# Performance work log

Hardware: AMD Instinct MI355X
Metric: run time of the kernel (lower is better)

Reference implementation:

```python
import jax, jax.numpy as jnp
import numpy as np

N_EMB = 1024
HEAD_SIZE = 128


def setup_inputs() -> dict:
    key = jax.random.key(0)
    k1, k2, k3, k4 = jax.random.split(key, 4)
    B, T = 8, 4096
    x = jax.random.normal(k1, (B, T, N_EMB), dtype=jnp.float32)
    # nn.Linear(n_emb, head_size, bias=False) weights have shape [head_size, n_emb]
    s = 1.0 / np.sqrt(N_EMB)
    Wq = jax.random.uniform(k2, (HEAD_SIZE, N_EMB), jnp.float32, -s, s)
    Wk = jax.random.uniform(k3, (HEAD_SIZE, N_EMB), jnp.float32, -s, s)
    Wv = jax.random.uniform(k4, (HEAD_SIZE, N_EMB), jnp.float32, -s, s)
    return {"x": x, "Wq": Wq, "Wk": Wk, "Wv": Wv}


def reference(x, Wq, Wk, Wv):
    # x: [B, T, C]; W*: [H, C]
    B, T, C = x.shape
    H = Wq.shape[0]
    q = jnp.einsum('btc,hc->bth', x, Wq)
    k = jnp.einsum('btc,hc->bth', x, Wk)
    v = jnp.einsum('btc,hc->bth', x, Wv)
    scale = H ** -0.5
    wei = jnp.einsum('bth,bsh->bts', q, k) * scale  # [B, T, T]
    # causal mask: position t attends to s <= t
    causal = jnp.arange(T)[:, None] >= jnp.arange(T)[None, :]
    wei = jnp.where(causal, wei, -jnp.inf)
    wei = jax.nn.softmax(wei, axis=-1)
    # dropout treated as identity (eval mode)
    out = jnp.einsum('bts,bsh->bth', wei, v)  # [B, T, H]
    return out
```

## Files before the change

kernel.cpp:

```cpp
#include <hip/hip_runtime.h>
#include <hip/hip_bf16.h>

typedef __bf16 bf16_t;
typedef __attribute__((ext_vector_type(8))) __bf16 bf16x8;
typedef __attribute__((ext_vector_type(4))) __bf16 bf16x4;
typedef __attribute__((ext_vector_type(4))) float f32x4;

#define MFMA16(a, b, c) __builtin_amdgcn_mfma_f32_16x16x32_bf16((a), (b), (c), 0, 0, 0)

__device__ __forceinline__ void gload_lds16(const void* g, void* l) {
    __builtin_amdgcn_global_load_lds(
        (const __attribute__((address_space(1))) void*)g,
        (__attribute__((address_space(3))) void*)l, 16, 0, 0);
}

__global__ __launch_bounds__(256, 3) void proj_qkv(
    const float* __restrict__ X,
    const float* __restrict__ W0, const float* __restrict__ W1, const float* __restrict__ W2,
    bf16_t* __restrict__ O0, bf16_t* __restrict__ O1, bf16_t* __restrict__ O2)
{
    __shared__ __align__(16) char As[128 * 128];
    __shared__ __align__(16) char Bs[128 * 128];

    const int tid = threadIdx.x;
    const int wid = tid >> 6;
    const int lane = tid & 63;
    const int l15 = lane & 15, l4 = lane >> 4;
    const int wr = wid >> 1, wc = wid & 1;
    const int m0 = blockIdx.x * 128;

    const float* W = (blockIdx.y == 0) ? W0 : (blockIdx.y == 1 ? W1 : W2);

    const int r0 = tid >> 4;
    const int kq = tid & 15;
    const int swz = ((r0 & 7) << 4);

    f32x4 acc[4][4] = {};
    float4 xr[8];

    #pragma unroll
    for (int i = 0; i < 8; ++i)
        xr[i] = *(const float4*)(X + (size_t)(m0 + r0 + i * 16) * 1024 + kq * 4);

    for (int ks = 0; ks < 16; ++ks) {
        const int kb = ks * 64;
        #pragma unroll
        for (int i = 0; i < 8; ++i) {
            const int r = r0 + i * 16;
            bf16x4 av; av[0] = (bf16_t)xr[i].x; av[1] = (bf16_t)xr[i].y;
            av[2] = (bf16_t)xr[i].z; av[3] = (bf16_t)xr[i].w;
            *(bf16x4*)(As + r * 128 + ((kq * 8) ^ swz)) = av;
        }
        #pragma unroll
        for (int i = 0; i < 8; ++i) {
            const int r = r0 + i * 16;
            float4 wa = *(const float4*)(W + (size_t)r * 1024 + kb + kq * 4);
            bf16x4 wv; wv[0] = (bf16_t)wa.x; wv[1] = (bf16_t)wa.y;
            wv[2] = (bf16_t)wa.z; wv[3] = (bf16_t)wa.w;
            *(bf16x4*)(Bs + r * 128 + ((kq * 8) ^ swz)) = wv;
        }
        __syncthreads();
        if (ks < 15) {
            #pragma unroll
            for (int i = 0; i < 8; ++i)
                xr[i] = *(const float4*)(X + (size_t)(m0 + r0 + i * 16) * 1024 + kb + 64 + kq * 4);
        }
        #pragma unroll
        for (int kk = 0; kk < 64; kk += 32) {
            const int kbyte = 2 * kk + 16 * l4;
            bf16x8 af[4], bfr[4];
            #pragma unroll
            for (int mi = 0; mi < 4; ++mi) {
                int r = wr * 64 + mi * 16 + l15;
                af[mi] = *(const bf16x8*)(As + r * 128 + (kbyte ^ ((r & 7) << 4)));
            }
            #pragma unroll
            for (int ni = 0; ni < 4; ++ni) {
                int r = wc * 64 + ni * 16 + l15;
                bfr[ni] = *(const bf16x8*)(Bs + r * 128 + (kbyte ^ ((r & 7) << 4)));
            }
            #pragma unroll
            for (int mi = 0; mi < 4; ++mi)
                #pragma unroll
                for (int ni = 0; ni < 4; ++ni)
                    acc[mi][ni] = MFMA16(af[mi], bfr[ni], acc[mi][ni]);
        }
        __syncthreads();
    }

    if (blockIdx.y < 2) {
        const float sc = (blockIdx.y == 0) ? 0.12751754816f : 1.0f;
        bf16_t* O = (blockIdx.y == 0) ? O0 : O1;
        #pragma unroll
        for (int mi = 0; mi < 4; ++mi)
            #pragma unroll
            for (int ni = 0; ni < 4; ++ni) {
                int row = m0 + wr * 64 + mi * 16 + l4 * 4;
                int col = wc * 64 + ni * 16 + l15;
                #pragma unroll
                for (int r = 0; r < 4; ++r)
                    O[(size_t)(row + r) * 128 + col] = (bf16_t)(acc[mi][ni][r] * sc);
            }
    } else {
        #pragma unroll
        for (int mi = 0; mi < 4; ++mi)
            #pragma unroll
            for (int ni = 0; ni < 4; ++ni) {
                int row0 = m0 + wr * 64 + mi * 16 + l4 * 4;
                int col = wc * 64 + ni * 16 + l15;
                int bb = row0 >> 12, t0 = row0 & 4095;
                bf16x4 pk;
                #pragma unroll
                for (int r = 0; r < 4; ++r) pk[r] = (bf16_t)acc[mi][ni][r];
                *(bf16x4*)(O2 + ((size_t)bb << 19) + (size_t)col * 4096 + t0) = pk;
            }
    }
}

__global__ __launch_bounds__(256, 2) void attn_fwd(
    const bf16_t* __restrict__ Qb, const bf16_t* __restrict__ Kb,
    const bf16_t* __restrict__ Vtg, float* __restrict__ out, int Bn)
{
    __shared__ __align__(16) char lds[73728];

    const int tid = threadIdx.x, wid = tid >> 6, lane = tid & 63;
    const int l15 = lane & 15, l4 = lane >> 4;

    const int blk = blockIdx.x;
    const int b = blk % Bn;
    const int j = blk / Bn;

    const size_t base = (size_t)b * 4096 * 128;
    const size_t baseVT = (size_t)b << 19;

    char* Vw = lds + wid * 16384;
    char* Pw = lds + 65536 + wid * 2048;
    const int pswz = (l15 >> 1) & 3;
    const int vswz = (l15 >> 1) & 3;

    const int sh = lane >> 2;
    const int skb = (((lane & 3) ^ ((sh >> 1) & 3))) * 8;

    for (int seg = 0; seg < 2; ++seg) {
        const int p = seg ? (127 - j) : j;
        const int q0 = p << 5;
        const int nt = (p >= wid) ? ((p - wid) >> 2) + 1 : 0;

        bf16x8 aq[2][4];
        #pragma unroll
        for (int qs = 0; qs < 2; ++qs)
            #pragma unroll
            for (int kf = 0; kf < 4; ++kf)
                aq[qs][kf] = *(const bf16x8*)(Qb + base
                    + (size_t)(q0 + 16 * qs + l15) * 128 + 32 * kf + 8 * l4);

        float mx[2] = {-1e30f, -1e30f}, lsum[2] = {0.f, 0.f};
        f32x4 o[2][8] = {};
        bf16x8 kreg[2][4];

        auto stageV = [&](int i) {
            const int kv0 = (wid + 4 * i) << 5;
            char* dst = Vw + (i & 1) * 8192;
            #pragma unroll
            for (int c = 0; c < 8; ++c) {
                const bf16_t* src = Vtg + baseVT + (size_t)(16 * c + sh) * 4096 + kv0 + skb;
                gload_lds16(src, dst + c * 1024);
            }
        };
        auto loadK = [&](int i) {
            const int kv0 = (wid + 4 * i) << 5;
            const bf16_t* kp = Kb + base + (size_t)(kv0 + l15) * 128 + 8 * l4;
            #pragma unroll
            for (int ni = 0; ni < 2; ++ni)
                #pragma unroll
                for (int kf = 0; kf < 4; ++kf)
                    kreg[ni][kf] = *(const bf16x8*)(kp + (size_t)ni * 2048 + kf * 32);
        };

        if (nt > 0) { loadK(0); stageV(0); }

        for (int i = 0; i < nt; ++i) {
            const int lt = wid + 4 * i;
            const int kv0 = lt << 5;

            f32x4 sa[2][2];
            #pragma unroll
            for (int qs = 0; qs < 2; ++qs)
                #pragma unroll
                for (int ni = 0; ni < 2; ++ni) sa[qs][ni] = (f32x4){0.f, 0.f, 0.f, 0.f};
            __builtin_amdgcn_s_setprio(1);
            #pragma unroll
            for (int kf = 0; kf < 4; ++kf)
                #pragma unroll
                for (int ni = 0; ni < 2; ++ni) {
                    sa[0][ni] = MFMA16(kreg[ni][kf], aq[0][kf], sa[0][ni]);
                    sa[1][ni] = MFMA16(kreg[ni][kf], aq[1][kf], sa[1][ni]);
                }
            __builtin_amdgcn_s_setprio(0);

            if (i + 1 < nt) loadK(i + 1);

            if (lt == p) {
                #pragma unroll
                for (int qs = 0; qs < 2; ++qs) {
                    const int qg = q0 + 16 * qs + l15;
                    #pragma unroll
                    for (int ni = 0; ni < 2; ++ni)
                        #pragma unroll
                        for (int r = 0; r < 4; ++r)
                            if (kv0 + 16 * ni + 4 * l4 + r > qg) sa[qs][ni][r] = -1e30f;
                }
            }

            #pragma unroll
            for (int qs = 0; qs < 2; ++qs) {
                float tm = sa[qs][0][0];
                #pragma unroll
                for (int ni = 0; ni < 2; ++ni)
                    #pragma unroll
                    for (int r = 0; r < 4; ++r) tm = fmaxf(tm, sa[qs][ni][r]);
                tm = fmaxf(tm, __shfl_xor(tm, 16, 64));
                tm = fmaxf(tm, __shfl_xor(tm, 32, 64));
                if (__any(tm > mx[qs])) {
                    const float mnew = fmaxf(mx[qs], tm);
                    const float c = exp2f(mx[qs] - mnew);
                    lsum[qs] *= c;
                    #pragma unroll
                    for (int mf = 0; mf < 8; ++mf) {
                        f32x4 t = o[qs][mf];
                        t[0] *= c; t[1] *= c; t[2] *= c; t[3] *= c;
                        o[qs][mf] = t;
                    }
                    mx[qs] = mnew;
                }
                float ss = 0.f;
                #pragma unroll
                for (int ni = 0; ni < 2; ++ni)
                    #pragma unroll
                    for (int r = 0; r < 4; ++r) {
                        float pv = exp2f(sa[qs][ni][r] - mx[qs]);
                        sa[qs][ni][r] = pv;
                        ss += pv;
                    }
                ss += __shfl_xor(ss, 16, 64);
                ss += __shfl_xor(ss, 32, 64);
                lsum[qs] += ss;
                #pragma unroll
                for (int ni = 0; ni < 2; ++ni) {
                    bf16x4 pv;
                    pv[0] = (bf16_t)sa[qs][ni][0]; pv[1] = (bf16_t)sa[qs][ni][1];
                    pv[2] = (bf16_t)sa[qs][ni][2]; pv[3] = (bf16_t)sa[qs][ni][3];
                    *(bf16x4*)(Pw + (16 * qs + l15) * 64
                               + (((2 * ni + (l4 >> 1)) ^ pswz) << 4) + 8 * (l4 & 1)) = pv;
                }
            }

            __builtin_amdgcn_sched_barrier(0);
            asm volatile("s_waitcnt vmcnt(8)" ::: "memory");
            __builtin_amdgcn_sched_barrier(0);

            char* Vbuf = Vw + (i & 1) * 8192;
            bf16x8 pa0 = *(const bf16x8*)(Pw + l15 * 64 + ((l4 ^ pswz) << 4));
            bf16x8 pa1 = *(const bf16x8*)(Pw + (16 + l15) * 64 + ((l4 ^ pswz) << 4));
            __builtin_amdgcn_s_setprio(1);
            #pragma unroll
            for (int mf = 0; mf < 8; ++mf) {
                bf16x8 av = *(const bf16x8*)(Vbuf + (16 * mf + l15) * 64
                                             + ((l4 ^ vswz) << 4));
                o[0][mf] = MFMA16(av, pa0, o[0][mf]);
                o[1][mf] = MFMA16(av, pa1, o[1][mf]);
            }
            __builtin_amdgcn_s_setprio(0);

            if (i + 1 < nt) stageV(i + 1);
        }

        asm volatile("s_waitcnt vmcnt(0)" ::: "memory");
        __syncthreads();
        #pragma unroll
        for (int qs = 0; qs < 2; ++qs)
            #pragma unroll
            for (int mf = 0; mf < 8; ++mf)
                *(f32x4*)(lds + wid * 16384 + (qs * 8 + mf) * 1024 + lane * 16) = o[qs][mf];
        if (l4 == 0) {
            #pragma unroll
            for (int qs = 0; qs < 2; ++qs)
                *(float2*)(lds + 65536 + wid * 256 + (qs * 16 + l15) * 8)
                    = make_float2(mx[qs], lsum[qs]);
        }
        __syncthreads();
        #pragma unroll
        for (int qs = 0; qs < 2; ++qs) {
            float mw[4], lw[4];
            #pragma unroll
            for (int w = 0; w < 4; ++w) {
                float2 st = *(const float2*)(lds + 65536 + w * 256 + (qs * 16 + l15) * 8);
                mw[w] = st.x; lw[w] = st.y;
            }
            const float M = fmaxf(fmaxf(mw[0], mw[1]), fmaxf(mw[2], mw[3]));
            float cw[4], L = 0.f;
            #pragma unroll
            for (int w = 0; w < 4; ++w) { cw[w] = exp2f(mw[w] - M); L += lw[w] * cw[w]; }
            const float inv = 1.f / L;
            #pragma unroll
            for (int mm = 0; mm < 2; ++mm) {
                const int mf = 2 * wid + mm;
                f32x4 acc = (f32x4){0.f, 0.f, 0.f, 0.f};
                #pragma unroll
                for (int w = 0; w < 4; ++w) {
                    f32x4 v = *(const f32x4*)(lds + w * 16384 + (qs * 8 + mf) * 1024 + lane * 16);
                    #pragma unroll
                    for (int e = 0; e < 4; ++e) acc[e] += v[e] * cw[w];
                }
                #pragma unroll
                for (int e = 0; e < 4; ++e) acc[e] *= inv;
                float* op = out + ((size_t)b * 4096 + q0 + 16 * qs + l15) * 128 + 16 * mf + 4 * l4;
                *(f32x4*)op = acc;
            }
        }
        __syncthreads();
    }
}

extern "C" void kernel_launch(void* const* d_in, const int* in_sizes, int n_in,
                              void* d_out, int out_size, void* d_ws, size_t ws_size,
                              hipStream_t stream) {
    const float* X  = (const float*)d_in[0];
    const float* Wq = (const float*)d_in[1];
    const float* Wk = (const float*)d_in[2];
    const float* Wv = (const float*)d_in[3];
    float* out = (float*)d_out;

    const int M = in_sizes[0] / 1024;
    const int Bn = M / 4096;

    bf16_t* Qb  = (bf16_t*)d_ws;
    bf16_t* KbP = Qb + (size_t)M * 128;
    bf16_t* VtP = KbP + (size_t)M * 128;

    proj_qkv<<<dim3(M / 128, 3), 256, 0, stream>>>(X, Wq, Wk, Wv, Qb, KbP, VtP);
    attn_fwd<<<dim3(64 * Bn), 256, 0, stream>>>(Qb, KbP, VtP, out, Bn);
}
```

Before: 137.7 us.

## Compute softmax row sums with ones-MFMA and lazily rescale running max

Replaces the per-tile VALU sum plus cross-lane shuffles for the softmax denominator with an extra MFMA against a vector of bf16 ones, so the row sum accumulates in matrix units from the same bf16 P values used in PV. It also skips the max reduction shuffles and rescaling unless some score exceeds the running max by more than 8 (log2 domain), tolerating exponentials up to 2^8 before rescale. This cuts VALU and shuffle work in the softmax inner loop. The risk lies in bf16 rounding of the denominator and larger intermediate P values, which affect accuracy.

```diff
diff --git a/kernel.cpp b/kernel.cpp
--- a/kernel.cpp
+++ b/kernel.cpp
@@ -141,6 +141,10 @@
     const int sh = lane >> 2;
     const int skb = (((lane & 3) ^ ((sh >> 1) & 3))) * 8;
 
+    bf16x8 aones;
+    #pragma unroll
+    for (int e = 0; e < 8; ++e) aones[e] = (bf16_t)1.0f;
+
     for (int seg = 0; seg < 2; ++seg) {
         const int p = seg ? (127 - j) : j;
         const int q0 = p << 5;
@@ -154,7 +158,8 @@
                 aq[qs][kf] = *(const bf16x8*)(Qb + base
                     + (size_t)(q0 + 16 * qs + l15) * 128 + 32 * kf + 8 * l4);
 
-        float mx[2] = {-1e30f, -1e30f}, lsum[2] = {0.f, 0.f};
+        float mx[2] = {-1e30f, -1e30f};
+        f32x4 ls_acc[2] = {};
         f32x4 o[2][8] = {};
         bf16x8 kreg[2][4];
 
@@ -214,17 +219,18 @@
 
             #pragma unroll
             for (int qs = 0; qs < 2; ++qs) {
-                float tm = sa[qs][0][0];
-                #pragma unroll
-                for (int ni = 0; ni < 2; ++ni)
-                    #pragma unroll
-                    for (int r = 0; r < 4; ++r) tm = fmaxf(tm, sa[qs][ni][r]);
-                tm = fmaxf(tm, __shfl_xor(tm, 16, 64));
-                tm = fmaxf(tm, __shfl_xor(tm, 32, 64));
-                if (__any(tm > mx[qs])) {
+                float tm = fmaxf(fmaxf(fmaxf(sa[qs][0][0], sa[qs][0][1]),
+                                       fmaxf(sa[qs][0][2], sa[qs][0][3])),
+                                 fmaxf(fmaxf(sa[qs][1][0], sa[qs][1][1]),
+                                       fmaxf(sa[qs][1][2], sa[qs][1][3])));
+                if (__any(tm > mx[qs] + 8.0f)) {
+                    tm = fmaxf(tm, __shfl_xor(tm, 16, 64));
+                    tm = fmaxf(tm, __shfl_xor(tm, 32, 64));
                     const float mnew = fmaxf(mx[qs], tm);
                     const float c = exp2f(mx[qs] - mnew);
-                    lsum[qs] *= c;
+                    f32x4 lt4 = ls_acc[qs];
+                    lt4[0] *= c; lt4[1] *= c; lt4[2] *= c; lt4[3] *= c;
+                    ls_acc[qs] = lt4;
                     #pragma unroll
                     for (int mf = 0; mf < 8; ++mf) {
                         f32x4 t = o[qs][mf];
@@ -233,23 +239,12 @@
                     }
                     mx[qs] = mnew;
                 }
-                float ss = 0.f;
-                #pragma unroll
-                for (int ni = 0; ni < 2; ++ni)
-                    #pragma unroll
-                    for (int r = 0; r < 4; ++r) {
-                        float pv = exp2f(sa[qs][ni][r] - mx[qs]);
-                        sa[qs][ni][r] = pv;
-                        ss += pv;
-                    }
-                ss += __shfl_xor(ss, 16, 64);
-                ss += __shfl_xor(ss, 32, 64);
-                lsum[qs] += ss;
                 #pragma unroll
                 for (int ni = 0; ni < 2; ++ni) {
                     bf16x4 pv;
-                    pv[0] = (bf16_t)sa[qs][ni][0]; pv[1] = (bf16_t)sa[qs][ni][1];
-                    pv[2] = (bf16_t)sa[qs][ni][2]; pv[3] = (bf16_t)sa[qs][ni][3];
+                    #pragma unroll
+                    for (int r = 0; r < 4; ++r)
+                        pv[r] = (bf16_t)exp2f(sa[qs][ni][r] - mx[qs]);
                     *(bf16x4*)(Pw + (16 * qs + l15) * 64
                                + (((2 * ni + (l4 >> 1)) ^ pswz) << 4) + 8 * (l4 & 1)) = pv;
                 }
@@ -263,6 +258,8 @@
             bf16x8 pa0 = *(const bf16x8*)(Pw + l15 * 64 + ((l4 ^ pswz) << 4));
             bf16x8 pa1 = *(const bf16x8*)(Pw + (16 + l15) * 64 + ((l4 ^ pswz) << 4));
             __builtin_amdgcn_s_setprio(1);
+            ls_acc[0] = MFMA16(aones, pa0, ls_acc[0]);
+            ls_acc[1] = MFMA16(aones, pa1, ls_acc[1]);
             #pragma unroll
             for (int mf = 0; mf < 8; ++mf) {
                 bf16x8 av = *(const bf16x8*)(Vbuf + (16 * mf + l15) * 64
@@ -286,7 +283,7 @@
             #pragma unroll
             for (int qs = 0; qs < 2; ++qs)
                 *(float2*)(lds + 65536 + wid * 256 + (qs * 16 + l15) * 8)
-                    = make_float2(mx[qs], lsum[qs]);
+                    = make_float2(mx[qs], ls_acc[qs][0]);
         }
         __syncthreads();
         #pragma unroll
```

New measurement: 137.4 us. No clear change (-0.2%).
